# Performance work log

Measured on AMD Instinct MI355X. Metric: run time of the kernel, lower is better.

Reference implementation:

```python
import jax, jax.numpy as jnp
import numpy as np

B, T, NH, EX, VOCAB, NLAYER = 8, 510, 12, 768, 256, 6
NBLK = 2 * NLAYER - 1          # 11 blocks, all with out=ex
NE = T + 2                     # CustomEmb output dim = n_embd = 512
HD = EX // NH
EXIT_SCALE = 1.0 / float(np.sqrt(4 * NBLK))  # torch init divides 'exit' params by sqrt(#exit params)


def _ln(x, s, b):
    m = jnp.mean(x, axis=-1, keepdims=True)
    v = jnp.mean((x - m) ** 2, axis=-1, keepdims=True)
    return (x - m) * jax.lax.rsqrt(v + 1e-5) * s + b


def setup_inputs() -> dict:
    key = jax.random.key(0)
    ks = iter(jax.random.split(key, 40))
    def n(shape, scale=0.02):
        return jax.random.normal(next(ks), shape, jnp.float32) * scale
    inp = {}
    inp['idx'] = jax.random.randint(next(ks), (B, T), 0, 2)
    inp['lin_w'] = n((NE, EX)); inp['lin_b'] = n((EX,))
    # stacked per-block params (leading dim NBLK), torch Linear math y = x @ W + b with W stored (in,out)
    inp['ln1_s'] = jnp.ones((NBLK, EX), jnp.float32); inp['ln1_b'] = jnp.zeros((NBLK, EX), jnp.float32)
    inp['qw'] = n((NBLK, EX, EX)); inp['qb'] = n((NBLK, EX))
    inp['kw'] = n((NBLK, EX, EX)); inp['kb'] = n((NBLK, EX))
    inp['vw'] = n((NBLK, EX, EX)); inp['vb'] = n((NBLK, EX))
    inp['ew'] = n((NBLK, EX, EX)) * EXIT_SCALE; inp['eb'] = n((NBLK, EX)) * EXIT_SCALE
    inp['ln2_s'] = jnp.ones((NBLK, EX), jnp.float32); inp['ln2_b'] = jnp.zeros((NBLK, EX), jnp.float32)
    inp['m1w'] = n((NBLK, EX, 4 * EX)); inp['m1b'] = n((NBLK, 4 * EX))
    inp['m2w'] = n((NBLK, 4 * EX, EX)) * EXIT_SCALE; inp['m2b'] = n((NBLK, EX)) * EXIT_SCALE
    inp['lnf_s'] = jnp.ones((EX,), jnp.float32); inp['lnf_b'] = jnp.zeros((EX,), jnp.float32)
    inp['head_w'] = n((EX * T, VOCAB)); inp['head_b'] = n((VOCAB,))
    return inp


def reference(idx, lin_w, lin_b, ln1_s, ln1_b, qw, qb, kw, kb, vw, vb, ew, eb,
              ln2_s, ln2_b, m1w, m1b, m2w, m2b, lnf_s, lnf_b, head_w, head_b):
    # CustomEmb: one-hot of binary token + identity positional encoding -> [B,T,T+2]
    e0 = (idx == 0).astype(jnp.float32)
    e1 = (idx == 1).astype(jnp.float32)
    pos = jnp.broadcast_to(jnp.eye(T, dtype=jnp.float32), (B, T, T))
    x = jnp.concatenate([e0[:, :, None], e1[:, :, None], pos], axis=2)
    x = jax.nn.relu(x @ lin_w + lin_b)                       # [B,T,EX]
    mask = jnp.tril(jnp.ones((T, T), bool))
    inv_sqrt_d = 1.0 / float(np.sqrt(HD))

    def block(x, p):
        l1s, l1b, Qw, Qb, Kw, Kb, Vw, Vb, Ew, Eb, l2s, l2b, M1w, M1b, M2w, M2b = p
        h = _ln(x, l1s, l1b)
        q = (h @ Qw + Qb).reshape(B, T, NH, HD)
        k = (h @ Kw + Kb).reshape(B, T, NH, HD)
        v = (h @ Vw + Vb).reshape(B, T, NH, HD)
        att = jnp.einsum('bqhd,bkhd->bhqk', q, k) * inv_sqrt_d
        att = jnp.where(mask, att, -jnp.inf)
        probs = jax.nn.softmax(att, axis=-1)
        y = jnp.einsum('bhqk,bkhd->bqhd', probs, v).reshape(B, T, EX)
        x = x + y @ Ew + Eb
        h2 = _ln(x, l2s, l2b)
        x = x + jax.nn.relu(h2 @ M1w + M1b) @ M2w + M2b      # MLP depth=2: initial+relu+exit
        return x, None

    x, _ = jax.lax.scan(block, x, (ln1_s, ln1_b, qw, qb, kw, kb, vw, vb,
                                   ew, eb, ln2_s, ln2_b, m1w, m1b, m2w, m2b))
    x = _ln(x, lnf_s, lnf_b)
    return x.reshape(B, -1) @ head_w + head_b                # [B, VOCAB]
```

## Files before the change

kernel.cpp:

```cpp
#include <hip/hip_runtime.h>
#include <hip/hip_bf16.h>
#include <math.h>

constexpr int cB = 8, cT = 510, cNH = 12, cEX = 768, cVOC = 256, cNBLK = 11, cHD = 64;
constexpr int cMB = 512;
constexpr int cMP = 4096;
constexpr int cQKV = 3 * cEX;

typedef __attribute__((ext_vector_type(8))) short bf16x8;
typedef __attribute__((ext_vector_type(4))) float f32x4;
using bf16 = __hip_bfloat16;

__device__ inline void gload16(const void* g, void* l) {
    __builtin_amdgcn_global_load_lds((const __attribute__((address_space(1))) unsigned int*)g,
                                     (__attribute__((address_space(3))) unsigned int*)l, 16, 0, 0);
}
__device__ inline short f2bs(float f) {
    bf16 b = __float2bfloat16(f);
    return *reinterpret_cast<short*>(&b);
}

__global__ __launch_bounds__(256) void embed_kernel(
    const int* __restrict__ idx, const float* __restrict__ lin_w,
    const float* __restrict__ lin_b, float* __restrict__ x)
{
    int row = blockIdx.x;
    int b = row >> 9, t = row & 511;
    float* xr = x + (size_t)row * cEX;
    if (t >= cT) {
        for (int j = threadIdx.x; j < cEX; j += 256) xr[j] = 0.0f;
        return;
    }
    int tok = idx[b * cT + t] & 1;
    const float* wt = lin_w + (size_t)tok * cEX;
    const float* wp = lin_w + (size_t)(2 + t) * cEX;
    for (int j = threadIdx.x; j < cEX; j += 256) {
        float val = wt[j] + wp[j] + lin_b[j];
        xr[j] = fmaxf(val, 0.0f);
    }
}

template<typename OUT>
__global__ __launch_bounds__(256) void ln_wave(
    const float* __restrict__ in, const float* __restrict__ s,
    const float* __restrict__ bsh, OUT* __restrict__ out)
{
    const int wid = threadIdx.x >> 6, lane = threadIdx.x & 63;
    const int row = blockIdx.x * 4 + wid;
    const float* xr = in + (size_t)row * cEX;
    float4 v[3];
    float sum = 0.f, sq = 0.f;
#pragma unroll
    for (int p = 0; p < 3; ++p) {
        v[p] = *(const float4*)&xr[p * 256 + lane * 4];
        sum += v[p].x + v[p].y + v[p].z + v[p].w;
        sq  += v[p].x * v[p].x + v[p].y * v[p].y + v[p].z * v[p].z + v[p].w * v[p].w;
    }
#pragma unroll
    for (int off = 1; off < 64; off <<= 1) {
        sum += __shfl_xor(sum, off, 64);
        sq  += __shfl_xor(sq, off, 64);
    }
    float mean = sum * (1.0f / cEX);
    float var = sq * (1.0f / cEX) - mean * mean;
    float rstd = rsqrtf(var + 1e-5f);
    OUT* outr = out + (size_t)row * cEX;
#pragma unroll
    for (int p = 0; p < 3; ++p) {
        int c = p * 256 + lane * 4;
        float4 sv = *(const float4*)&s[c];
        float4 bv = *(const float4*)&bsh[c];
        float o0 = (v[p].x - mean) * rstd * sv.x + bv.x;
        float o1 = (v[p].y - mean) * rstd * sv.y + bv.y;
        float o2 = (v[p].z - mean) * rstd * sv.z + bv.z;
        float o3 = (v[p].w - mean) * rstd * sv.w + bv.w;
        if constexpr (sizeof(OUT) == 2) {
            short4 pk;
            pk.x = f2bs(o0); pk.y = f2bs(o1); pk.z = f2bs(o2); pk.w = f2bs(o3);
            *(short4*)&outr[c] = pk;
        } else {
            *(float4*)&outr[c] = make_float4(o0, o1, o2, o3);
        }
    }
}

__global__ __launch_bounds__(256) void transpose_w(
    const float* __restrict__ W, bf16* __restrict__ WT,
    int K, int N, size_t w_stride, size_t wt_stride, int wt_row_off)
{
    __shared__ float t[32][33];
    const float* Wb = W + (size_t)blockIdx.z * w_stride;
    bf16* WTb = WT + (size_t)blockIdx.z * wt_stride;
    int n0 = blockIdx.x * 32, k0 = blockIdx.y * 32;
    int c = threadIdx.x & 31, ty = threadIdx.x >> 5;
#pragma unroll
    for (int it = 0; it < 4; ++it) {
        int r = ty + it * 8;
        t[r][c] = Wb[(size_t)(k0 + r) * N + n0 + c];
    }
    __syncthreads();
#pragma unroll
    for (int it = 0; it < 4; ++it) {
        int a = ty + it * 8;
        WTb[(size_t)(wt_row_off + n0 + a) * K + k0 + c] = __float2bfloat16(t[c][a]);
    }
}

__global__ __launch_bounds__(256) void concat_bias(
    const float* __restrict__ qb, const float* __restrict__ kb,
    const float* __restrict__ vb, float* __restrict__ qkvb)
{
    int i = blockIdx.x * 256 + threadIdx.x;
    if (i >= cNBLK * cQKV) return;
    int blk = i / cQKV, c = i - blk * cQKV;
    const float* src; int cc = c;
    if (c < cEX)            { src = qb; }
    else if (c < 2 * cEX)   { src = kb; cc = c - cEX; }
    else                    { src = vb; cc = c - 2 * cEX; }
    qkvb[i] = src[(size_t)blk * cEX + cc];
}

template<int FM, int FN, bool RELU, bool RESID, bool OUTBF16, bool VT>
__global__ __launch_bounds__(256) void gemm_db(
    const short* __restrict__ A, const short* __restrict__ BT,
    const float* __restrict__ bias, const float* __restrict__ resid,
    void* __restrict__ Cout, short* __restrict__ vTr, int K, int N)
{
    constexpr int BM = FM * 32, BN = FN * 32;
    constexpr int TS = (BM + BN) * 64;
    constexpr int CA = BM / 32, CB = BN / 32;
    constexpr int LPT = CA + CB;
    __shared__ short lds[2 * TS];
    const int tid = threadIdx.x;
    const int lane = tid & 63, wid = tid >> 6;
    const int wm = wid >> 1, wn = wid & 1;
    const int bm = blockIdx.y * BM, bn = blockIdx.x * BN;
    const int li = lane & 15, gk = lane >> 4;

    f32x4 acc[FM][FN];
#pragma unroll
    for (int i = 0; i < FM; ++i)
#pragma unroll
        for (int j = 0; j < FN; ++j)
            acc[i][j] = f32x4{0.f, 0.f, 0.f, 0.f};

    auto stage = [&](int kt, int buf) {
        short* la = &lds[buf * TS];
        short* lb = la + BM * 64;
#pragma unroll
        for (int i = 0; i < CA; ++i) {
            int s = i * 256 + tid;
            int r = s >> 3, c = s & 7;
            gload16(A + (size_t)(bm + r) * K + kt * 64 + (c ^ (r & 7)) * 8,
                    (char*)la + (size_t)(i * 256 + wid * 64) * 16);
        }
#pragma unroll
        for (int i = 0; i < CB; ++i) {
            int s = i * 256 + tid;
            int r = s >> 3, c = s & 7;
            gload16(BT + (size_t)(bn + r) * K + kt * 64 + (c ^ (r & 7)) * 8,
                    (char*)lb + (size_t)(i * 256 + wid * 64) * 16);
        }
    };

    const int nkt = K >> 6;
    stage(0, 0);
    stage(1, 1);

    for (int t = 0; t < nkt; ++t) {
        if (t + 1 < nkt) {
            if constexpr (LPT == 8) asm volatile("s_waitcnt vmcnt(8)" ::: "memory");
            else                    asm volatile("s_waitcnt vmcnt(6)" ::: "memory");
        } else {
            asm volatile("s_waitcnt vmcnt(0)" ::: "memory");
        }
        __builtin_amdgcn_s_barrier();

        const short* la = &lds[(t & 1) * TS];
        const short* lb = la + BM * 64;

        bf16x8 af0[FM], bf0[FN];
#pragma unroll
        for (int mi = 0; mi < FM; ++mi) {
            int row = wm * FM * 16 + mi * 16 + li;
            af0[mi] = *(const bf16x8*)&la[row * 64 + (gk ^ (row & 7)) * 8];
        }
#pragma unroll
        for (int ni = 0; ni < FN; ++ni) {
            int row = wn * FN * 16 + ni * 16 + li;
            bf0[ni] = *(const bf16x8*)&lb[row * 64 + (gk ^ (row & 7)) * 8];
        }
        __builtin_amdgcn_s_setprio(1);
#pragma unroll
        for (int mi = 0; mi < FM; ++mi)
#pragma unroll
            for (int ni = 0; ni < FN; ++ni)
                acc[mi][ni] = __builtin_amdgcn_mfma_f32_16x16x32_bf16(
                    af0[mi], bf0[ni], acc[mi][ni], 0, 0, 0);
        __builtin_amdgcn_s_setprio(0);

        bf16x8 af1[FM], bf1[FN];
#pragma unroll
        for (int mi = 0; mi < FM; ++mi) {
            int row = wm * FM * 16 + mi * 16 + li;
            af1[mi] = *(const bf16x8*)&la[row * 64 + ((4 + gk) ^ (row & 7)) * 8];
        }
#pragma unroll
        for (int ni = 0; ni < FN; ++ni) {
            int row = wn * FN * 16 + ni * 16 + li;
            bf1[ni] = *(const bf16x8*)&lb[row * 64 + ((4 + gk) ^ (row & 7)) * 8];
        }
        asm volatile("s_waitcnt lgkmcnt(0)" ::: "memory");
        __builtin_amdgcn_s_barrier();
        if (t + 2 < nkt) stage(t + 2, t & 1);
        __builtin_amdgcn_s_setprio(1);
#pragma unroll
        for (int mi = 0; mi < FM; ++mi)
#pragma unroll
            for (int ni = 0; ni < FN; ++ni)
                acc[mi][ni] = __builtin_amdgcn_mfma_f32_16x16x32_bf16(
                    af1[mi], bf1[ni], acc[mi][ni], 0, 0, 0);
        __builtin_amdgcn_s_setprio(0);
    }

#pragma unroll
    for (int mi = 0; mi < FM; ++mi) {
#pragma unroll
        for (int ni = 0; ni < FN; ++ni) {
            int col = bn + wn * FN * 16 + ni * 16 + li;
            float bv = bias[col];
            int row0 = bm + wm * FM * 16 + mi * 16 + gk * 4;
            if (VT && col >= 2 * cEX) {
                short4 pk;
                pk.x = f2bs(acc[mi][ni][0] + bv);
                pk.y = f2bs(acc[mi][ni][1] + bv);
                pk.z = f2bs(acc[mi][ni][2] + bv);
                pk.w = f2bs(acc[mi][ni][3] + bv);
                *(short4*)&vTr[(size_t)(col - 2 * cEX) * cMP + row0] = pk;
            } else {
#pragma unroll
                for (int j = 0; j < 4; ++j) {
                    int row = row0 + j;
                    float v = acc[mi][ni][j] + bv;
                    if (RELU) v = fmaxf(v, 0.0f);
                    if (RESID) v += resid[(size_t)row * N + col];
                    if (OUTBF16)
                        ((bf16*)Cout)[(size_t)row * N + col] = __float2bfloat16(v);
                    else
                        ((float*)Cout)[(size_t)row * N + col] = v;
                }
            }
        }
    }
}

__global__ __launch_bounds__(256) void attn_mfma(
    const short* __restrict__ qkv, const short* __restrict__ vT, bf16* __restrict__ y)
{
    const int qt = blockIdx.x, h = blockIdx.y, b = blockIdx.z;
    __shared__ short Ks[64 * 64];
    __shared__ short Vs[64 * 64];
    __shared__ short Ss[4][16][72];
    const int tid = threadIdx.x;
    const int lane = tid & 63, wid = tid >> 6;
    const int li = lane & 15, gk = lane >> 4;

    const size_t rowb = (size_t)b * cMB;
    int qr = qt * 64 + wid * 16 + li;
    int qrc = qr < cT ? qr : cT - 1;
    const short* qrow = qkv + (rowb + qrc) * cQKV + h * cHD;
    bf16x8 qf0 = *(const bf16x8*)(qrow + gk * 8);
    bf16x8 qf1 = *(const bf16x8*)(qrow + 32 + gk * 8);

    f32x4 o[4];
    float mrow[4], lrow[4];
#pragma unroll
    for (int dt = 0; dt < 4; ++dt) o[dt] = f32x4{0.f, 0.f, 0.f, 0.f};
#pragma unroll
    for (int j = 0; j < 4; ++j) { mrow[j] = -3e38f; lrow[j] = 0.f; }

    const int qloc = qt * 64 + wid * 16 + gk * 4;

    const int nkt = qt + 1;
    for (int kt = 0; kt < nkt; ++kt) {
#pragma unroll
        for (int i = 0; i < 2; ++i) {
            int s = i * 256 + tid;
            int r = s >> 3, c = s & 7;
            gload16(qkv + (rowb + kt * 64 + r) * cQKV + cEX + h * cHD + (c ^ (r & 7)) * 8,
                    (char*)Ks + (size_t)(i * 256 + wid * 64) * 16);
        }
#pragma unroll
        for (int i = 0; i < 2; ++i) {
            int s = i * 256 + tid;
            int d = s >> 3, c = s & 7;
            gload16(vT + (size_t)(h * cHD + d) * cMP + rowb + kt * 64 + (c ^ (d & 7)) * 8,
                    (char*)Vs + (size_t)(i * 256 + wid * 64) * 16);
        }
        __syncthreads();

        f32x4 sg[4];
#pragma unroll
        for (int g = 0; g < 4; ++g) sg[g] = f32x4{0.f, 0.f, 0.f, 0.f};
#pragma unroll
        for (int g = 0; g < 4; ++g) {
            int key = g * 16 + li;
            bf16x8 k0 = *(const bf16x8*)&Ks[key * 64 + (gk ^ (key & 7)) * 8];
            bf16x8 k1 = *(const bf16x8*)&Ks[key * 64 + ((4 + gk) ^ (key & 7)) * 8];
            sg[g] = __builtin_amdgcn_mfma_f32_16x16x32_bf16(qf0, k0, sg[g], 0, 0, 0);
            sg[g] = __builtin_amdgcn_mfma_f32_16x16x32_bf16(qf1, k1, sg[g], 0, 0, 0);
        }

#pragma unroll
        for (int j = 0; j < 4; ++j) {
            int q = qloc + j;
            float sc[4];
#pragma unroll
            for (int g = 0; g < 4; ++g) {
                int kg = kt * 64 + g * 16 + li;
                sc[g] = (kg <= q) ? sg[g][j] * 0.125f : -3e38f;
            }
            float tm = fmaxf(fmaxf(sc[0], sc[1]), fmaxf(sc[2], sc[3]));
            tm = fmaxf(tm, __shfl_xor(tm, 1, 16));
            tm = fmaxf(tm, __shfl_xor(tm, 2, 16));
            tm = fmaxf(tm, __shfl_xor(tm, 4, 16));
            tm = fmaxf(tm, __shfl_xor(tm, 8, 16));
            float mnew = fmaxf(mrow[j], tm);
            float p[4], ps = 0.f;
#pragma unroll
            for (int g = 0; g < 4; ++g) { p[g] = __expf(sc[g] - mnew); ps += p[g]; }
            ps += __shfl_xor(ps, 1, 16);
            ps += __shfl_xor(ps, 2, 16);
            ps += __shfl_xor(ps, 4, 16);
            ps += __shfl_xor(ps, 8, 16);
            float scale = __expf(mrow[j] - mnew);
            lrow[j] = lrow[j] * scale + ps;
            mrow[j] = mnew;
#pragma unroll
            for (int dt = 0; dt < 4; ++dt) o[dt][j] *= scale;
#pragma unroll
            for (int g = 0; g < 4; ++g)
                Ss[wid][gk * 4 + j][g * 16 + li] = f2bs(p[g]);
        }

        bf16x8 pa0 = *(const bf16x8*)&Ss[wid][li][gk * 8];
        bf16x8 pa1 = *(const bf16x8*)&Ss[wid][li][32 + gk * 8];
#pragma unroll
        for (int dt = 0; dt < 4; ++dt) {
            int d = dt * 16 + li;
            bf16x8 vf0 = *(const bf16x8*)&Vs[d * 64 + (gk ^ (d & 7)) * 8];
            bf16x8 vf1 = *(const bf16x8*)&Vs[d * 64 + ((4 + gk) ^ (d & 7)) * 8];
            o[dt] = __builtin_amdgcn_mfma_f32_16x16x32_bf16(pa0, vf0, o[dt], 0, 0, 0);
            o[dt] = __builtin_amdgcn_mfma_f32_16x16x32_bf16(pa1, vf1, o[dt], 0, 0, 0);
        }
        __syncthreads();
    }

#pragma unroll
    for (int j = 0; j < 4; ++j) {
        int q = qloc + j;
        if (q >= cT) continue;
        float inv = 1.0f / lrow[j];
        bf16* yr = y + (rowb + q) * cEX + h * cHD;
#pragma unroll
        for (int dt = 0; dt < 4; ++dt)
            yr[dt * 16 + li] = __float2bfloat16(o[dt][j] * inv);
    }
}

__global__ __launch_bounds__(256) void head_part_kernel(
    const float* __restrict__ xf, const float* __restrict__ hw, float* __restrict__ part)
{
    __shared__ float xs[8][1536];
    const int tid = threadIdx.x;
    const int k0 = blockIdx.x * 1536;
    for (int i = tid; i < 8 * 1536; i += 256) {
        int bb = i / 1536, kk = i - bb * 1536;
        xs[bb][kk] = xf[(size_t)bb * (cMB * cEX) + k0 + kk];
    }
    __syncthreads();
    float acc[8] = {};
    const float* wp = hw + (size_t)k0 * cVOC + tid;
    for (int kk = 0; kk < 1536; ++kk) {
        float w = wp[(size_t)kk * cVOC];
#pragma unroll
        for (int bb = 0; bb < 8; ++bb) acc[bb] += xs[bb][kk] * w;
    }
#pragma unroll
    for (int bb = 0; bb < 8; ++bb)
        part[((size_t)blockIdx.x * 8 + bb) * cVOC + tid] = acc[bb];
}

__global__ __launch_bounds__(256) void head_reduce_kernel(
    const float* __restrict__ part, const float* __restrict__ hb, float* __restrict__ out)
{
    int i = blockIdx.x * 256 + threadIdx.x;
    int bb = i >> 8, vv = i & 255;
    float acc = hb[vv];
    for (int c = 0; c < 255; ++c) acc += part[((size_t)c * 8 + bb) * 256 + vv];
    out[i] = acc;
}

extern "C" void kernel_launch(void* const* d_in, const int* in_sizes, int n_in,
                              void* d_out, int out_size, void* d_ws, size_t ws_size,
                              hipStream_t stream) {
    (void)in_sizes; (void)n_in; (void)out_size; (void)ws_size;
    const int*   idx    = (const int*)d_in[0];
    const float* lin_w  = (const float*)d_in[1];
    const float* lin_b  = (const float*)d_in[2];
    const float* ln1_s  = (const float*)d_in[3];
    const float* ln1_b  = (const float*)d_in[4];
    const float* qw     = (const float*)d_in[5];
    const float* qbias  = (const float*)d_in[6];
    const float* kw     = (const float*)d_in[7];
    const float* kbias  = (const float*)d_in[8];
    const float* vw     = (const float*)d_in[9];
    const float* vbias  = (const float*)d_in[10];
    const float* ew     = (const float*)d_in[11];
    const float* ebias  = (const float*)d_in[12];
    const float* ln2_s  = (const float*)d_in[13];
    const float* ln2_b  = (const float*)d_in[14];
    const float* m1w    = (const float*)d_in[15];
    const float* m1b    = (const float*)d_in[16];
    const float* m2w    = (const float*)d_in[17];
    const float* m2b    = (const float*)d_in[18];
    const float* lnf_s  = (const float*)d_in[19];
    const float* lnf_b  = (const float*)d_in[20];
    const float* head_w = (const float*)d_in[21];
    const float* head_b = (const float*)d_in[22];
    float* out = (float*)d_out;

    const size_t act = (size_t)cMP * cEX;
    float* x    = (float*)d_ws;
    float* xf   = x + act;
    float* part = xf + act;
    float* qkvb = part + 255 * 8 * 256;
    short* qkv  = (short*)(qkvb + cNBLK * cQKV);
    short* vTr  = qkv + (size_t)cMP * cQKV;
    short* h    = vTr + (size_t)cEX * cMP;
    short* h2   = h + act;
    short* y    = h2 + act;
    short* u    = y + act;
    short* wqkvT = u + (size_t)cMP * 4 * cEX;
    short* weT   = wqkvT + (size_t)cNBLK * cQKV * cEX;
    short* wm1T  = weT + (size_t)cNBLK * cEX * cEX;
    short* wm2T  = wm1T + (size_t)cNBLK * cEX * 4 * cEX;

    transpose_w<<<dim3(24, 24, cNBLK), 256, 0, stream>>>(qw, (bf16*)wqkvT, cEX, cEX,
        (size_t)cEX * cEX, (size_t)cQKV * cEX, 0);
    transpose_w<<<dim3(24, 24, cNBLK), 256, 0, stream>>>(kw, (bf16*)wqkvT, cEX, cEX,
        (size_t)cEX * cEX, (size_t)cQKV * cEX, cEX);
    transpose_w<<<dim3(24, 24, cNBLK), 256, 0, stream>>>(vw, (bf16*)wqkvT, cEX, cEX,
        (size_t)cEX * cEX, (size_t)cQKV * cEX, 2 * cEX);
    transpose_w<<<dim3(24, 24, cNBLK), 256, 0, stream>>>(ew, (bf16*)weT, cEX, cEX,
        (size_t)cEX * cEX, (size_t)cEX * cEX, 0);
    transpose_w<<<dim3(96, 24, cNBLK), 256, 0, stream>>>(m1w, (bf16*)wm1T, cEX, 4 * cEX,
        (size_t)cEX * 4 * cEX, (size_t)cEX * 4 * cEX, 0);
    transpose_w<<<dim3(24, 96, cNBLK), 256, 0, stream>>>(m2w, (bf16*)wm2T, 4 * cEX, cEX,
        (size_t)cEX * 4 * cEX, (size_t)cEX * 4 * cEX, 0);
    concat_bias<<<(cNBLK * cQKV + 255) / 256, 256, 0, stream>>>(qbias, kbias, vbias, qkvb);

    embed_kernel<<<cMP, 256, 0, stream>>>(idx, lin_w, lin_b, x);

    for (int blk = 0; blk < cNBLK; ++blk) {
        size_t bo = (size_t)blk * cEX;
        ln_wave<bf16><<<cMP / 4, 256, 0, stream>>>(x, ln1_s + bo, ln1_b + bo, (bf16*)h);
        gemm_db<4, 4, false, false, true, true><<<dim3(cQKV / 128, cMP / 128), 256, 0, stream>>>(
            h, wqkvT + (size_t)blk * cQKV * cEX, qkvb + (size_t)blk * cQKV, nullptr,
            qkv, vTr, cEX, cQKV);
        attn_mfma<<<dim3(8, cNH, cB), 256, 0, stream>>>(qkv, vTr, (bf16*)y);
        gemm_db<2, 4, false, true, false, false><<<dim3(cEX / 128, cMP / 64), 256, 0, stream>>>(
            y, weT + (size_t)blk * cEX * cEX, ebias + bo, x, x, nullptr, cEX, cEX);
        ln_wave<bf16><<<cMP / 4, 256, 0, stream>>>(x, ln2_s + bo, ln2_b + bo, (bf16*)h2);
        gemm_db<4, 4, true, false, true, false><<<dim3(4 * cEX / 128, cMP / 128), 256, 0, stream>>>(
            h2, wm1T + (size_t)blk * cEX * 4 * cEX, m1b + (size_t)blk * 4 * cEX, nullptr,
            u, nullptr, cEX, 4 * cEX);
        gemm_db<2, 4, false, true, false, false><<<dim3(cEX / 128, cMP / 64), 256, 0, stream>>>(
            u, wm2T + (size_t)blk * cEX * 4 * cEX, m2b + bo, x, x, nullptr, 4 * cEX, cEX);
    }
    ln_wave<float><<<cMP / 4, 256, 0, stream>>>(x, lnf_s, lnf_b, xf);
    head_part_kernel<<<255, 256, 0, stream>>>(xf, head_w, part);
    head_reduce_kernel<<<8, 256, 0, stream>>>(part, head_b, out);
}
```

Before: 1.794 ms.

## Enlarge GEMM tiles with 8 waves, swizzle grid, double-buffer attention, fuse final LN

Result: slower. 1.874 ms (+4.4%).

```diff
diff --git a/kernel.cpp b/kernel.cpp
--- a/kernel.cpp
+++ b/kernel.cpp
@@ -120,21 +120,25 @@
     qkvb[i] = src[(size_t)blk * cEX + cc];
 }
 
-template<int FM, int FN, bool RELU, bool RESID, bool OUTBF16, bool VT>
-__global__ __launch_bounds__(256) void gemm_db(
+template<int WM, int WN, int FM, int FN, bool RELU, bool RESID, bool OUTBF16, bool VT>
+__global__ __launch_bounds__(WM * WN * 64) void gemm_db(
     const short* __restrict__ A, const short* __restrict__ BT,
     const float* __restrict__ bias, const float* __restrict__ resid,
     void* __restrict__ Cout, short* __restrict__ vTr, int K, int N)
 {
-    constexpr int BM = FM * 32, BN = FN * 32;
+    constexpr int T = WM * WN * 64;
+    constexpr int BM = WM * FM * 16, BN = WN * FN * 16;
     constexpr int TS = (BM + BN) * 64;
-    constexpr int CA = BM / 32, CB = BN / 32;
+    constexpr int CA = BM * 8 / T, CB = BN * 8 / T;
     constexpr int LPT = CA + CB;
     __shared__ short lds[2 * TS];
     const int tid = threadIdx.x;
     const int lane = tid & 63, wid = tid >> 6;
-    const int wm = wid >> 1, wn = wid & 1;
-    const int bm = blockIdx.y * BM, bn = blockIdx.x * BN;
+    const int wm = wid / WN, wn = wid % WN;
+    int nwg = gridDim.x * gridDim.y;
+    int wg = blockIdx.y * gridDim.x + blockIdx.x;
+    int swz = (wg & 7) * (nwg >> 3) + (wg >> 3);
+    const int bm = (swz / gridDim.x) * BM, bn = (swz % gridDim.x) * BN;
     const int li = lane & 15, gk = lane >> 4;
 
     f32x4 acc[FM][FN];
@@ -149,17 +153,17 @@
         short* lb = la + BM * 64;
 #pragma unroll
         for (int i = 0; i < CA; ++i) {
-            int s = i * 256 + tid;
+            int s = i * T + tid;
             int r = s >> 3, c = s & 7;
             gload16(A + (size_t)(bm + r) * K + kt * 64 + (c ^ (r & 7)) * 8,
-                    (char*)la + (size_t)(i * 256 + wid * 64) * 16);
+                    (char*)la + (size_t)(i * T + wid * 64) * 16);
         }
 #pragma unroll
         for (int i = 0; i < CB; ++i) {
-            int s = i * 256 + tid;
+            int s = i * T + tid;
             int r = s >> 3, c = s & 7;
             gload16(BT + (size_t)(bn + r) * K + kt * 64 + (c ^ (r & 7)) * 8,
-                    (char*)lb + (size_t)(i * 256 + wid * 64) * 16);
+                    (char*)lb + (size_t)(i * T + wid * 64) * 16);
         }
     };
 
@@ -182,12 +186,12 @@
         bf16x8 af0[FM], bf0[FN];
 #pragma unroll
         for (int mi = 0; mi < FM; ++mi) {
-            int row = wm * FM * 16 + mi * 16 + li;
+            int row = (wm * FM + mi) * 16 + li;
             af0[mi] = *(const bf16x8*)&la[row * 64 + (gk ^ (row & 7)) * 8];
         }
 #pragma unroll
         for (int ni = 0; ni < FN; ++ni) {
-            int row = wn * FN * 16 + ni * 16 + li;
+            int row = (wn * FN + ni) * 16 + li;
             bf0[ni] = *(const bf16x8*)&lb[row * 64 + (gk ^ (row & 7)) * 8];
         }
         __builtin_amdgcn_s_setprio(1);
@@ -202,12 +206,12 @@
         bf16x8 af1[FM], bf1[FN];
 #pragma unroll
         for (int mi = 0; mi < FM; ++mi) {
-            int row = wm * FM * 16 + mi * 16 + li;
+            int row = (wm * FM + mi) * 16 + li;
             af1[mi] = *(const bf16x8*)&la[row * 64 + ((4 + gk) ^ (row & 7)) * 8];
         }
 #pragma unroll
         for (int ni = 0; ni < FN; ++ni) {
-            int row = wn * FN * 16 + ni * 16 + li;
+            int row = (wn * FN + ni) * 16 + li;
             bf1[ni] = *(const bf16x8*)&lb[row * 64 + ((4 + gk) ^ (row & 7)) * 8];
         }
         asm volatile("s_waitcnt lgkmcnt(0)" ::: "memory");
@@ -227,9 +231,9 @@
     for (int mi = 0; mi < FM; ++mi) {
 #pragma unroll
         for (int ni = 0; ni < FN; ++ni) {
-            int col = bn + wn * FN * 16 + ni * 16 + li;
+            int col = bn + (wn * FN + ni) * 16 + li;
             float bv = bias[col];
-            int row0 = bm + wm * FM * 16 + mi * 16 + gk * 4;
+            int row0 = bm + (wm * FM + mi) * 16 + gk * 4;
             if (VT && col >= 2 * cEX) {
                 short4 pk;
                 pk.x = f2bs(acc[mi][ni][0] + bv);
@@ -258,8 +262,8 @@
     const short* __restrict__ qkv, const short* __restrict__ vT, bf16* __restrict__ y)
 {
     const int qt = blockIdx.x, h = blockIdx.y, b = blockIdx.z;
-    __shared__ short Ks[64 * 64];
-    __shared__ short Vs[64 * 64];
+    __shared__ short Ks[2][64 * 64];
+    __shared__ short Vs[2][64 * 64];
     __shared__ short Ss[4][16][72];
     const int tid = threadIdx.x;
     const int lane = tid & 63, wid = tid >> 6;
@@ -281,23 +285,34 @@
 
     const int qloc = qt * 64 + wid * 16 + gk * 4;
 
-    const int nkt = qt + 1;
-    for (int kt = 0; kt < nkt; ++kt) {
+    auto stage = [&](int kt, int buf) {
 #pragma unroll
         for (int i = 0; i < 2; ++i) {
             int s = i * 256 + tid;
             int r = s >> 3, c = s & 7;
             gload16(qkv + (rowb + kt * 64 + r) * cQKV + cEX + h * cHD + (c ^ (r & 7)) * 8,
-                    (char*)Ks + (size_t)(i * 256 + wid * 64) * 16);
+                    (char*)&Ks[buf][0] + (size_t)(i * 256 + wid * 64) * 16);
         }
 #pragma unroll
         for (int i = 0; i < 2; ++i) {
             int s = i * 256 + tid;
             int d = s >> 3, c = s & 7;
             gload16(vT + (size_t)(h * cHD + d) * cMP + rowb + kt * 64 + (c ^ (d & 7)) * 8,
-                    (char*)Vs + (size_t)(i * 256 + wid * 64) * 16);
-        }
-        __syncthreads();
+                    (char*)&Vs[buf][0] + (size_t)(i * 256 + wid * 64) * 16);
+        }
+    };
+
+    const int nkt = qt + 1;
+    stage(0, 0);
+    for (int kt = 0; kt < nkt; ++kt) {
+        if (kt + 1 < nkt) {
+            stage(kt + 1, (kt + 1) & 1);
+            asm volatile("s_waitcnt vmcnt(4)" ::: "memory");
+        } else {
+            asm volatile("s_waitcnt vmcnt(0)" ::: "memory");
+        }
+        __builtin_amdgcn_s_barrier();
+        const int cur = kt & 1;
 
         f32x4 sg[4];
 #pragma unroll
@@ -305,8 +320,8 @@
 #pragma unroll
         for (int g = 0; g < 4; ++g) {
             int key = g * 16 + li;
-            bf16x8 k0 = *(const bf16x8*)&Ks[key * 64 + (gk ^ (key & 7)) * 8];
-            bf16x8 k1 = *(const bf16x8*)&Ks[key * 64 + ((4 + gk) ^ (key & 7)) * 8];
+            bf16x8 k0 = *(const bf16x8*)&Ks[cur][key * 64 + (gk ^ (key & 7)) * 8];
+            bf16x8 k1 = *(const bf16x8*)&Ks[cur][key * 64 + ((4 + gk) ^ (key & 7)) * 8];
             sg[g] = __builtin_amdgcn_mfma_f32_16x16x32_bf16(qf0, k0, sg[g], 0, 0, 0);
             sg[g] = __builtin_amdgcn_mfma_f32_16x16x32_bf16(qf1, k1, sg[g], 0, 0, 0);
         }
@@ -348,12 +363,13 @@
 #pragma unroll
         for (int dt = 0; dt < 4; ++dt) {
             int d = dt * 16 + li;
-            bf16x8 vf0 = *(const bf16x8*)&Vs[d * 64 + (gk ^ (d & 7)) * 8];
-            bf16x8 vf1 = *(const bf16x8*)&Vs[d * 64 + ((4 + gk) ^ (d & 7)) * 8];
+            bf16x8 vf0 = *(const bf16x8*)&Vs[cur][d * 64 + (gk ^ (d & 7)) * 8];
+            bf16x8 vf1 = *(const bf16x8*)&Vs[cur][d * 64 + ((4 + gk) ^ (d & 7)) * 8];
             o[dt] = __builtin_amdgcn_mfma_f32_16x16x32_bf16(pa0, vf0, o[dt], 0, 0, 0);
             o[dt] = __builtin_amdgcn_mfma_f32_16x16x32_bf16(pa1, vf1, o[dt], 0, 0, 0);
         }
-        __syncthreads();
+        asm volatile("s_waitcnt lgkmcnt(0)" ::: "memory");
+        __builtin_amdgcn_s_barrier();
     }
 
 #pragma unroll
@@ -369,17 +385,50 @@
 }
 
 __global__ __launch_bounds__(256) void head_part_kernel(
-    const float* __restrict__ xf, const float* __restrict__ hw, float* __restrict__ part)
+    const float* __restrict__ x, const float* __restrict__ lnf_s,
+    const float* __restrict__ lnf_b, const float* __restrict__ hw,
+    float* __restrict__ part)
 {
     __shared__ float xs[8][1536];
+    __shared__ float stat[16][2];
     const int tid = threadIdx.x;
-    const int k0 = blockIdx.x * 1536;
+    const int trow0 = blockIdx.x * 2;
+    const int wid = tid >> 6, lane = tid & 63;
+    {
+        const int g = lane >> 4, li = lane & 15;
+        const int p = wid * 4 + g, bb = p >> 1, rr = p & 1;
+        const float* xr = x + ((size_t)(bb * cMB + trow0 + rr)) * cEX;
+        float sum = 0.f, sq = 0.f;
+#pragma unroll
+        for (int it = 0; it < 12; ++it) {
+            float4 v = *(const float4*)&xr[it * 64 + li * 4];
+            sum += v.x + v.y + v.z + v.w;
+            sq  += v.x * v.x + v.y * v.y + v.z * v.z + v.w * v.w;
+        }
+#pragma unroll
+        for (int off = 8; off > 0; off >>= 1) {
+            sum += __shfl_xor(sum, off, 16);
+            sq  += __shfl_xor(sq, off, 16);
+        }
+        if (li == 0) {
+            float mean = sum * (1.0f / cEX);
+            float var = sq * (1.0f / cEX) - mean * mean;
+            stat[p][0] = mean;
+            stat[p][1] = rsqrtf(var + 1e-5f);
+        }
+    }
+    __syncthreads();
     for (int i = tid; i < 8 * 1536; i += 256) {
         int bb = i / 1536, kk = i - bb * 1536;
-        xs[bb][kk] = xf[(size_t)bb * (cMB * cEX) + k0 + kk];
+        int rr = kk >= cEX ? 1 : 0;
+        int e = kk - rr * cEX;
+        float mean = stat[bb * 2 + rr][0], rstd = stat[bb * 2 + rr][1];
+        float val = x[((size_t)(bb * cMB + trow0 + rr)) * cEX + e];
+        xs[bb][kk] = (val - mean) * rstd * lnf_s[e] + lnf_b[e];
     }
     __syncthreads();
     float acc[8] = {};
+    const int k0 = blockIdx.x * 1536;
     const float* wp = hw + (size_t)k0 * cVOC + tid;
     for (int kk = 0; kk < 1536; ++kk) {
         float w = wp[(size_t)kk * cVOC];
@@ -432,8 +481,7 @@
 
     const size_t act = (size_t)cMP * cEX;
     float* x    = (float*)d_ws;
-    float* xf   = x + act;
-    float* part = xf + act;
+    float* part = x + act;
     float* qkvb = part + 255 * 8 * 256;
     short* qkv  = (short*)(qkvb + cNBLK * cQKV);
     short* vTr  = qkv + (size_t)cMP * cQKV;
@@ -465,20 +513,19 @@
     for (int blk = 0; blk < cNBLK; ++blk) {
         size_t bo = (size_t)blk * cEX;
         ln_wave<bf16><<<cMP / 4, 256, 0, stream>>>(x, ln1_s + bo, ln1_b + bo, (bf16*)h);
-        gemm_db<4, 4, false, false, true, true><<<dim3(cQKV / 128, cMP / 128), 256, 0, stream>>>(
+        gemm_db<4, 2, 4, 4, false, false, true, true><<<dim3(cQKV / 128, cMP / 256), 512, 0, stream>>>(
             h, wqkvT + (size_t)blk * cQKV * cEX, qkvb + (size_t)blk * cQKV, nullptr,
             qkv, vTr, cEX, cQKV);
         attn_mfma<<<dim3(8, cNH, cB), 256, 0, stream>>>(qkv, vTr, (bf16*)y);
-        gemm_db<2, 4, false, true, false, false><<<dim3(cEX / 128, cMP / 64), 256, 0, stream>>>(
+        gemm_db<2, 2, 2, 4, false, true, false, false><<<dim3(cEX / 128, cMP / 64), 256, 0, stream>>>(
             y, weT + (size_t)blk * cEX * cEX, ebias + bo, x, x, nullptr, cEX, cEX);
         ln_wave<bf16><<<cMP / 4, 256, 0, stream>>>(x, ln2_s + bo, ln2_b + bo, (bf16*)h2);
-        gemm_db<4, 4, true, false, true, false><<<dim3(4 * cEX / 128, cMP / 128), 256, 0, stream>>>(
+        gemm_db<4, 2, 4, 4, true, false, true, false><<<dim3(4 * cEX / 128, cMP / 256), 512, 0, stream>>>(
             h2, wm1T + (size_t)blk * cEX * 4 * cEX, m1b + (size_t)blk * 4 * cEX, nullptr,
             u, nullptr, cEX, 4 * cEX);
-        gemm_db<2, 4, false, true, false, false><<<dim3(cEX / 128, cMP / 64), 256, 0, stream>>>(
+        gemm_db<2, 2, 2, 4, false, true, false, false><<<dim3(cEX / 128, cMP / 64), 256, 0, stream>>>(
             u, wm2T + (size_t)blk * cEX * 4 * cEX, m2b + bo, x, x, nullptr, 4 * cEX, cEX);
     }
-    ln_wave<float><<<cMP / 4, 256, 0, stream>>>(x, lnf_s, lnf_b, xf);
-    head_part_kernel<<<255, 256, 0, stream>>>(xf, head_w, part);
+    head_part_kernel<<<255, 256, 0, stream>>>(x, lnf_s, lnf_b, head_w, part);
     head_reduce_kernel<<<8, 256, 0, stream>>>(part, head_b, out);
 }
```
